# Performance work log

Measured on AMD Instinct MI355X. Metric: run time of the kernel, lower is better.

## Reference

```python
import jax, jax.numpy as jnp
import numpy as np

EMBED_DIM = 4096
NUM_HEADS = 32
NUM_KV_HEADS = 8
HEAD_DIM = EMBED_DIM // NUM_HEADS          # 128
Q_PER_KV = NUM_HEADS // NUM_KV_HEADS       # 4
KV_DIM = HEAD_DIM * NUM_KV_HEADS           # 1024
ROPE_BASE = 10000.0
ROTARY_DIM = HEAD_DIM                      # rotary_emb_dim = 128 (full head)


def setup_inputs() -> dict:
    key = jax.random.key(0)
    k1, k2, k3 = jax.random.split(key, 3)
    b, s = 2, 2048
    x = jax.random.normal(k1, (b, s, EMBED_DIM), dtype=jnp.float32)
    # torch nn.Linear weight layout: (out_features, in_features); scaled init
    wqkv_w = jax.random.normal(k2, (EMBED_DIM + 2 * KV_DIM, EMBED_DIM), dtype=jnp.float32) * (EMBED_DIM ** -0.5)
    wo_w = jax.random.normal(k3, (EMBED_DIM, EMBED_DIM), dtype=jnp.float32) * (EMBED_DIM ** -0.5)
    return {"x": x, "wqkv_w": wqkv_w, "wo_w": wo_w}


def _rope_cos_sin(seqlen, dtype):
    inv_freq = 1.0 / (ROPE_BASE ** (jnp.arange(0, ROTARY_DIM, 2, dtype=jnp.float32) / ROTARY_DIM))
    t = jnp.arange(seqlen, dtype=jnp.float32)
    freqs = jnp.outer(t, inv_freq)                 # (s, d/2)
    emb = jnp.concatenate([freqs, freqs], axis=-1)  # (s, d) — HF convention
    return jnp.cos(emb).astype(dtype), jnp.sin(emb).astype(dtype)


def _rotate_half(x):
    x1, x2 = jnp.split(x, 2, axis=-1)
    return jnp.concatenate([-x2, x1], axis=-1)


def _apply_rope(x, cos, sin):
    # x: (b, s, h, d); cos/sin: (s, d)
    c = cos[None, :, None, :]
    s_ = sin[None, :, None, :]
    return x * c + _rotate_half(x) * s_


def reference(x, wqkv_w, wo_w):
    b, s, _ = x.shape
    # packed QKV projection
    qkv = jnp.einsum("bse,fe->bsf", x, wqkv_w)
    # b s (h_kv * (q_per_kv + 2) * d) -> b s h_kv (q_per_kv+2) d
    qkv = qkv.reshape(b, s, NUM_KV_HEADS, Q_PER_KV + 2, HEAD_DIM)
    q = qkv[..., :Q_PER_KV, :].reshape(b, s, NUM_HEADS, HEAD_DIM)
    k = qkv[..., -2, :]   # (b, s, h_kv, d)
    v = qkv[..., -1, :]   # (b, s, h_kv, d)

    # RoPE (HF rotate_half impl, offsets = 0)
    cos, sin = _rope_cos_sin(s, x.dtype)
    q = _apply_rope(q, cos, sin)
    k = _apply_rope(k, cos, sin)

    # GQA: expand kv heads to match q heads
    k = jnp.repeat(k, Q_PER_KV, axis=2)   # (b, s, h, d)
    v = jnp.repeat(v, Q_PER_KV, axis=2)

    scale = HEAD_DIM ** -0.5
    scores = jnp.einsum("bqhd,bkhd->bhqk", q, k) * scale
    causal_mask = jnp.tril(jnp.ones((s, s), dtype=bool))
    scores = jnp.where(causal_mask[None, None], scores, jnp.finfo(scores.dtype).min)
    probs = jax.nn.softmax(scores, axis=-1)
    context = jnp.einsum("bhqk,bkhd->bqhd", probs, v)
    context = context.reshape(b, s, EMBED_DIM)
    return jnp.einsum("bse,fe->bsf", context, wo_w)
```

## Files before the change

### kernel.cpp

```cpp
#include <hip/hip_runtime.h>
#include <hip/hip_bf16.h>
#include <stdint.h>

typedef __hip_bfloat16 bf16;
typedef short bf16x8 __attribute__((ext_vector_type(8)));
typedef float f32x4 __attribute__((ext_vector_type(4)));

#define MFMA16(a, b, c) __builtin_amdgcn_mfma_f32_16x16x32_bf16((a), (b), (c), 0, 0, 0)

__device__ __forceinline__ void gload16(const void* g, void* l) {
  __builtin_amdgcn_global_load_lds((const __attribute__((address_space(1))) void*)g,
                                   (__attribute__((address_space(3))) void*)l,
                                   16, 0, 0);
}

__device__ __forceinline__ void stv(float* p, float v) { *p = v; }
__device__ __forceinline__ void stv(bf16* p, float v) { *p = __float2bfloat16(v); }

__global__ void cast_f32_bf16(const float* __restrict__ in, bf16* __restrict__ out,
                              long n) {
  const long stride = (long)gridDim.x * blockDim.x * 8;
  for (long i = ((long)blockIdx.x * blockDim.x + threadIdx.x) * 8; i < n; i += stride) {
    const float4 a = *(const float4*)&in[i];
    const float4 b = *(const float4*)&in[i + 4];
    bf16 t[8];
    t[0] = __float2bfloat16(a.x); t[1] = __float2bfloat16(a.y);
    t[2] = __float2bfloat16(a.z); t[3] = __float2bfloat16(a.w);
    t[4] = __float2bfloat16(b.x); t[5] = __float2bfloat16(b.y);
    t[6] = __float2bfloat16(b.z); t[7] = __float2bfloat16(b.w);
    *(bf16x8*)&out[i] = *(const bf16x8*)t;
  }
}

template <typename OutT>
__global__ __launch_bounds__(512, 2) void gemm256(const bf16* __restrict__ A,
                                                  const bf16* __restrict__ B,
                                                  OutT* __restrict__ C,
                                                  int M, int N, int K) {
  const int nbn = N >> 8;
  const int nwg = gridDim.x;
  const int wg = blockIdx.x;
  const int cpx = nwg >> 3;
  const int swz = (wg & 7) * cpx + (wg >> 3);
  const int bm = swz / nbn;
  const int bn = swz - bm * nbn;

  __shared__ bf16 As[2][256][64];
  __shared__ bf16 Bs[2][256][64];

  const int tid = threadIdx.x;
  const int wave = tid >> 6, lane = tid & 63;
  const int lo = lane & 15, hi = lane >> 4;
  const int wm = wave >> 2, wn = wave & 3;

  const bf16* Ag = A + (long)(bm * 256) * K;
  const bf16* Bg = B + (long)(bn * 256) * K;

  int srow[4]; int scol[4]; int sdst[4];
#pragma unroll
  for (int i = 0; i < 4; i++) {
    const int c = i * 512 + wave * 64 + lane;
    const int row = c >> 3, p = c & 7;
    srow[i] = row;
    scol[i] = (p ^ (row & 7)) * 8;
    sdst[i] = (i * 512 + wave * 64) * 8;
  }

  f32x4 acc[8][4] = {};
  const int NT = K >> 6;

#pragma unroll
  for (int p = 0; p < 2; p++) {
#pragma unroll
    for (int i = 0; i < 4; i++)
      gload16(Ag + (long)srow[i] * K + p * 64 + scol[i], &As[p][0][0] + sdst[i]);
#pragma unroll
    for (int i = 0; i < 4; i++)
      gload16(Bg + (long)srow[i] * K + p * 64 + scol[i], &Bs[p][0][0] + sdst[i]);
  }

#pragma unroll 1
  for (int t = 0; t < NT; ++t) {
    if (t >= NT - 1) asm volatile("s_waitcnt vmcnt(0)" ::: "memory");
    else             asm volatile("s_waitcnt vmcnt(8)" ::: "memory");
    __builtin_amdgcn_s_barrier();

    const bf16* Ab = &As[t & 1][0][0];
    const bf16* Bb = &Bs[t & 1][0][0];

#pragma unroll
    for (int ks = 0; ks < 2; ks++) {
      bf16x8 af[8], bfr[4];
#pragma unroll
      for (int m = 0; m < 8; m++) {
        const int row = wm * 128 + m * 16 + lo;
        af[m] = *(const bf16x8*)&Ab[row * 64 + ((ks * 4 + hi) ^ (lo & 7)) * 8];
      }
#pragma unroll
      for (int n = 0; n < 4; n++) {
        const int row = wn * 64 + n * 16 + lo;
        bfr[n] = *(const bf16x8*)&Bb[row * 64 + ((ks * 4 + hi) ^ (lo & 7)) * 8];
      }
      __builtin_amdgcn_s_setprio(1);
#pragma unroll
      for (int m = 0; m < 8; m++)
#pragma unroll
        for (int n = 0; n < 4; n++) acc[m][n] = MFMA16(af[m], bfr[n], acc[m][n]);
      __builtin_amdgcn_s_setprio(0);
    }

    asm volatile("s_waitcnt lgkmcnt(0)" ::: "memory");
    __builtin_amdgcn_s_barrier();

    if (t + 2 < NT) {
      const int kt = (t + 2) * 64;
      bf16* Ad = &As[t & 1][0][0];
      bf16* Bd = &Bs[t & 1][0][0];
#pragma unroll
      for (int i = 0; i < 4; i++)
        gload16(Ag + (long)srow[i] * K + kt + scol[i], Ad + sdst[i]);
#pragma unroll
      for (int i = 0; i < 4; i++)
        gload16(Bg + (long)srow[i] * K + kt + scol[i], Bd + sdst[i]);
    }
  }

  const long crow0 = (long)bm * 256 + wm * 128;
  const long ccol0 = (long)bn * 256 + wn * 64;
#pragma unroll
  for (int m = 0; m < 8; m++)
#pragma unroll
    for (int n = 0; n < 4; n++)
#pragma unroll
      for (int r = 0; r < 4; r++)
        stv(&C[(crow0 + m * 16 + hi * 4 + r) * (long)N + ccol0 + n * 16 + lo],
            acc[m][n][r]);
}

__global__ void rope_qk(bf16* __restrict__ qkv) {
  const int row = blockIdx.x;
  const int t = row & 2047;
  const float scale = 0.08838834764831845f;
  for (int p = threadIdx.x; p < 40 * 64; p += blockDim.x) {
    const int sh = p >> 6, j = p & 63;
    const int kvh = sh / 5, slot = sh - kvh * 5;
    const long base = (long)row * 6144 + kvh * 768 + slot * 128 + j;
    const float x1 = __bfloat162float(qkv[base]);
    const float x2 = __bfloat162float(qkv[base + 64]);
    const float inv = __expf(-(float)j * 0.14391156831212787f);
    const float ang = (float)t * inv;
    const float c = cosf(ang), s = sinf(ang);
    float o1 = x1 * c - x2 * s;
    float o2 = x2 * c + x1 * s;
    if (slot < 4) { o1 *= scale; o2 *= scale; }
    qkv[base] = __float2bfloat16(o1);
    qkv[base + 64] = __float2bfloat16(o2);
  }
}

__global__ void vtrans(const bf16* __restrict__ qkv, bf16* __restrict__ Vt) {
  const int tt = blockIdx.x, dd = blockIdx.y, bk = blockIdx.z;
  const int kvh = bk & 7, b = bk >> 3;
  __shared__ bf16 tile[64][65];
  const int tx = threadIdx.x, ty = threadIdx.y;
  const bf16* src = qkv + ((long)(b * 2048 + tt * 64)) * 6144 + kvh * 768 + 640 + dd * 64;
  for (int r = ty; r < 64; r += 4) tile[r][tx] = src[(long)r * 6144 + tx];
  __syncthreads();
  bf16* dst = Vt + ((long)bk * 128 + dd * 64) * 2048 + tt * 64;
  for (int r = ty; r < 64; r += 4) dst[(long)r * 2048 + tx] = tile[tx][r];
}

__global__ __launch_bounds__(256) void attn(const bf16* __restrict__ qkv,
                                            const bf16* __restrict__ Vt,
                                            bf16* __restrict__ Ctx) {
  const int lin = blockIdx.x;
  const int c = (lin & 7) * 64 + (lin >> 3);
  const int z = c & 31;
  const int kvh = (c >> 5) & 7;
  const int b = c >> 8;

  const int wave = threadIdx.x >> 6;
  const int lane = threadIdx.x & 63;
  const int h = kvh * 4 + wave;
  const int lo = lane & 15, hi = lane >> 4;

  const bf16* Qb = qkv + (long)b * 2048 * 6144 + kvh * 768 + wave * 128;
  const bf16* Kb = qkv + (long)b * 2048 * 6144 + kvh * 768 + 512;
  const bf16* Vb = Vt + ((long)(b * 8 + kvh)) * 128 * 2048;

  __shared__ bf16 Plds[4][32][40];

#pragma unroll 1
  for (int pass = 0; pass < 2; ++pass) {
    const int qw = pass ? 63 - z : z;
    const int q0 = qw * 32;

    bf16x8 qf[2][4];
#pragma unroll
    for (int qb = 0; qb < 2; qb++)
#pragma unroll
      for (int dc = 0; dc < 4; dc++)
        qf[qb][dc] =
            *(const bf16x8*)&Qb[(long)(q0 + qb * 16 + lo) * 6144 + dc * 32 + hi * 8];

    f32x4 acc[2][8] = {};
    float mrow[2][4], lrow[2][4];
#pragma unroll
    for (int qb = 0; qb < 2; qb++)
#pragma unroll
      for (int r = 0; r < 4; r++) {
        mrow[qb][r] = -1e30f;
        lrow[qb][r] = 0.0f;
      }

    for (int kt = 0; kt <= qw; ++kt) {
      const int k0 = kt * 32;
      f32x4 sacc[2][2] = {};
      __builtin_amdgcn_s_setprio(1);
#pragma unroll
      for (int kb = 0; kb < 2; kb++)
#pragma unroll
        for (int dc = 0; dc < 4; dc++) {
          const bf16x8 kf =
              *(const bf16x8*)&Kb[(long)(k0 + kb * 16 + lo) * 6144 + dc * 32 + hi * 8];
          sacc[0][kb] = MFMA16(qf[0][dc], kf, sacc[0][kb]);
          sacc[1][kb] = MFMA16(qf[1][dc], kf, sacc[1][kb]);
        }
      __builtin_amdgcn_s_setprio(0);

      if (kt == qw) {
#pragma unroll
        for (int qb = 0; qb < 2; qb++)
#pragma unroll
          for (int kb = 0; kb < 2; kb++) {
            const int q = q0 + qb * 16 + hi * 4;
            const int k = k0 + kb * 16 + lo;
#pragma unroll
            for (int r = 0; r < 4; r++)
              if (k > q + r) sacc[qb][kb][r] = -1e30f;
          }
      }

      float p[2][2][4];
      float sf[2][4];
#pragma unroll
      for (int qb = 0; qb < 2; qb++)
#pragma unroll
        for (int r = 0; r < 4; r++) {
          float pm = fmaxf(sacc[qb][0][r], sacc[qb][1][r]);
          pm = fmaxf(pm, __shfl_xor(pm, 1));
          pm = fmaxf(pm, __shfl_xor(pm, 2));
          pm = fmaxf(pm, __shfl_xor(pm, 4));
          pm = fmaxf(pm, __shfl_xor(pm, 8));
          const float mn = fmaxf(mrow[qb][r], pm);
          sf[qb][r] = __expf(mrow[qb][r] - mn);
          mrow[qb][r] = mn;
          float ps = 0.0f;
#pragma unroll
          for (int kb = 0; kb < 2; kb++) {
            p[qb][kb][r] = __expf(sacc[qb][kb][r] - mn);
            ps += p[qb][kb][r];
          }
          ps += __shfl_xor(ps, 1);
          ps += __shfl_xor(ps, 2);
          ps += __shfl_xor(ps, 4);
          ps += __shfl_xor(ps, 8);
          lrow[qb][r] = lrow[qb][r] * sf[qb][r] + ps;
        }

#pragma unroll
      for (int qb = 0; qb < 2; qb++)
#pragma unroll
        for (int dt = 0; dt < 8; dt++)
#pragma unroll
          for (int r = 0; r < 4; r++) acc[qb][dt][r] *= sf[qb][r];

#pragma unroll
      for (int qb = 0; qb < 2; qb++)
#pragma unroll
        for (int kb = 0; kb < 2; kb++)
#pragma unroll
          for (int r = 0; r < 4; r++)
            Plds[wave][qb * 16 + hi * 4 + r][kb * 16 + lo] = __float2bfloat16(p[qb][kb][r]);

      bf16x8 pa[2];
#pragma unroll
      for (int qb = 0; qb < 2; qb++)
        pa[qb] = *(const bf16x8*)&Plds[wave][qb * 16 + lo][hi * 8];

      __builtin_amdgcn_s_setprio(1);
#pragma unroll
      for (int dt = 0; dt < 8; dt++) {
        const bf16x8 vf = *(const bf16x8*)&Vb[(long)(dt * 16 + lo) * 2048 + k0 + hi * 8];
        acc[0][dt] = MFMA16(pa[0], vf, acc[0][dt]);
        acc[1][dt] = MFMA16(pa[1], vf, acc[1][dt]);
      }
      __builtin_amdgcn_s_setprio(0);
    }

#pragma unroll
    for (int qb = 0; qb < 2; qb++)
#pragma unroll
      for (int dt = 0; dt < 8; dt++)
#pragma unroll
        for (int r = 0; r < 4; r++) {
          const float o = acc[qb][dt][r] / lrow[qb][r];
          const long row = (long)b * 2048 + q0 + qb * 16 + hi * 4 + r;
          Ctx[row * 4096 + h * 128 + dt * 16 + lo] = __float2bfloat16(o);
        }
  }
}


extern "C" void kernel_launch(void* const* d_in, const int* in_sizes, int n_in,
                              void* d_out, int out_size, void* d_ws, size_t ws_size,
                              hipStream_t stream) {
  (void)in_sizes; (void)n_in; (void)out_size; (void)ws_size;
  const float* x = (const float*)d_in[0];
  const float* wqkv = (const float*)d_in[1];
  const float* wo = (const float*)d_in[2];
  float* out = (float*)d_out;

  const long NX = 4096L * 4096;
  const long NW1 = 6144L * 4096;

  const size_t XB_B = (size_t)NX * 2;
  const size_t WQ_B = (size_t)NW1 * 2;
  const size_t QKV_B = WQ_B;

  char* w = (char*)d_ws;
  bf16* xb = (bf16*)w;
  bf16* wqkvb = (bf16*)(w + XB_B);
  bf16* qkvp = (bf16*)(w + XB_B + WQ_B);
  bf16* Vtp = (bf16*)(w + XB_B + WQ_B + QKV_B);
  bf16* wob = xb;
  bf16* ctx = wqkvb;

  cast_f32_bf16<<<2048, 256, 0, stream>>>(x, xb, NX);
  cast_f32_bf16<<<2048, 256, 0, stream>>>(wqkv, wqkvb, NW1);

  gemm256<bf16><<<16 * 24, 512, 0, stream>>>(xb, wqkvb, qkvp, 4096, 6144, 4096);

  rope_qk<<<4096, 256, 0, stream>>>(qkvp);
  vtrans<<<dim3(32, 2, 16), dim3(64, 4), 0, stream>>>(qkvp, Vtp);

  cast_f32_bf16<<<2048, 256, 0, stream>>>(wo, wob, NX);

  attn<<<dim3(512), 256, 0, stream>>>(qkvp, Vtp, ctx);

  gemm256<float><<<16 * 16, 512, 0, stream>>>(ctx, wob, out, 4096, 4096, 4096);
}
```

Baseline: 728.5 us.

## Interleave GEMM global-to-LDS staging with four-phase MFMA clusters per K-tile

Reworks the bf16 GEMM main loop into four MFMA phases per 64-wide K tile. Each phase's LDS fragment reads overlap the issue of one half-tile global_load_lds, with barriers and sched_barriers between phases. The B tile for t+1 and the A tile for t+2 are staged on staggered schedules, and the vmcnt wait drops from 8 to 4. This is meant to spread memory traffic across the compute rather than bursting it after the MFMAs. The cost is more barriers per iteration and a subtle buffer-reuse ordering that could race if misordered.

Result: faster. 687.1 us (-5.7%).

```diff
diff --git a/kernel.cpp b/kernel.cpp
--- a/kernel.cpp
+++ b/kernel.cpp
@@ -56,74 +56,111 @@
   const bf16* Ag = A + (long)(bm * 256) * K;
   const bf16* Bg = B + (long)(bn * 256) * K;
 
-  int srow[4]; int scol[4]; int sdst[4];
-#pragma unroll
-  for (int i = 0; i < 4; i++) {
-    const int c = i * 512 + wave * 64 + lane;
-    const int row = c >> 3, p = c & 7;
-    srow[i] = row;
-    scol[i] = (p ^ (row & 7)) * 8;
-    sdst[i] = (i * 512 + wave * 64) * 8;
+  int srow[2], scol[2], sdst[2];
+#pragma unroll
+  for (int j = 0; j < 2; j++) {
+    const int c = j * 512 + tid;
+    const int row = c >> 3;
+    srow[j] = row;
+    scol[j] = ((c & 7) ^ (row & 7)) * 8;
+    sdst[j] = (j * 512 + wave * 64) * 8;
+  }
+
+#define STG(G, S, kt, h)                                                      \
+  {                                                                           \
+    _Pragma("unroll") for (int j = 0; j < 2; j++)                             \
+        gload16((G) + (long)((h)*128 + srow[j]) * K + (kt) + scol[j],         \
+                (S) + (h)*8192 + sdst[j]);                                    \
   }
 
   f32x4 acc[8][4] = {};
   const int NT = K >> 6;
 
-#pragma unroll
-  for (int p = 0; p < 2; p++) {
-#pragma unroll
-    for (int i = 0; i < 4; i++)
-      gload16(Ag + (long)srow[i] * K + p * 64 + scol[i], &As[p][0][0] + sdst[i]);
-#pragma unroll
-    for (int i = 0; i < 4; i++)
-      gload16(Bg + (long)srow[i] * K + p * 64 + scol[i], &Bs[p][0][0] + sdst[i]);
-  }
+  STG(Ag, &As[0][0][0], 0, 0); STG(Ag, &As[0][0][0], 0, 1);
+  STG(Bg, &Bs[0][0][0], 0, 0); STG(Bg, &Bs[0][0][0], 0, 1);
+  STG(Ag, &As[1][0][0], 64, 0); STG(Ag, &As[1][0][0], 64, 1);
 
 #pragma unroll 1
   for (int t = 0; t < NT; ++t) {
     if (t >= NT - 1) asm volatile("s_waitcnt vmcnt(0)" ::: "memory");
-    else             asm volatile("s_waitcnt vmcnt(8)" ::: "memory");
+    else             asm volatile("s_waitcnt vmcnt(4)" ::: "memory");
     __builtin_amdgcn_s_barrier();
 
     const bf16* Ab = &As[t & 1][0][0];
     const bf16* Bb = &Bs[t & 1][0][0];
-
-#pragma unroll
-    for (int ks = 0; ks < 2; ks++) {
-      bf16x8 af[8], bfr[4];
-#pragma unroll
-      for (int m = 0; m < 8; m++) {
-        const int row = wm * 128 + m * 16 + lo;
-        af[m] = *(const bf16x8*)&Ab[row * 64 + ((ks * 4 + hi) ^ (lo & 7)) * 8];
-      }
-#pragma unroll
-      for (int n = 0; n < 4; n++) {
-        const int row = wn * 64 + n * 16 + lo;
-        bfr[n] = *(const bf16x8*)&Bb[row * 64 + ((ks * 4 + hi) ^ (lo & 7)) * 8];
-      }
-      __builtin_amdgcn_s_setprio(1);
-#pragma unroll
-      for (int m = 0; m < 8; m++)
-#pragma unroll
-        for (int n = 0; n < 4; n++) acc[m][n] = MFMA16(af[m], bfr[n], acc[m][n]);
-      __builtin_amdgcn_s_setprio(0);
+    bf16* SAn = &As[t & 1][0][0];
+    bf16* SBn = &Bs[(t + 1) & 1][0][0];
+    const int kt1 = (t + 1) * 64, kt2 = (t + 2) * 64;
+    const bool s1 = (t + 1 < NT), s2 = (t + 2 < NT);
+    const int c0 = (hi ^ (lo & 7)) * 8;
+    const int c1 = ((4 + hi) ^ (lo & 7)) * 8;
+
+    bf16x8 a0[4], a1[4], a2[4], a3[4], b0[4], b1[4];
+
+#pragma unroll
+    for (int m = 0; m < 4; m++) {
+      const int row = (wm * 128 + m * 16 + lo) * 64;
+      a0[m] = *(const bf16x8*)&Ab[row + c0];
+      a1[m] = *(const bf16x8*)&Ab[row + c1];
     }
-
+#pragma unroll
+    for (int n = 0; n < 4; n++)
+      b0[n] = *(const bf16x8*)&Bb[(wn * 64 + n * 16 + lo) * 64 + c0];
+    if (s1) STG(Bg, SBn, kt1, 0);
+    __builtin_amdgcn_s_barrier();
     asm volatile("s_waitcnt lgkmcnt(0)" ::: "memory");
-    __builtin_amdgcn_s_barrier();
-
-    if (t + 2 < NT) {
-      const int kt = (t + 2) * 64;
-      bf16* Ad = &As[t & 1][0][0];
-      bf16* Bd = &Bs[t & 1][0][0];
-#pragma unroll
-      for (int i = 0; i < 4; i++)
-        gload16(Ag + (long)srow[i] * K + kt + scol[i], Ad + sdst[i]);
-#pragma unroll
-      for (int i = 0; i < 4; i++)
-        gload16(Bg + (long)srow[i] * K + kt + scol[i], Bd + sdst[i]);
+    __builtin_amdgcn_sched_barrier(0);
+    __builtin_amdgcn_s_setprio(1);
+#pragma unroll
+    for (int m = 0; m < 4; m++)
+#pragma unroll
+      for (int n = 0; n < 4; n++) acc[m][n] = MFMA16(a0[m], b0[n], acc[m][n]);
+    __builtin_amdgcn_s_setprio(0);
+    __builtin_amdgcn_s_barrier();
+
+#pragma unroll
+    for (int m = 0; m < 4; m++) {
+      const int row = (wm * 128 + 64 + m * 16 + lo) * 64;
+      a2[m] = *(const bf16x8*)&Ab[row + c0];
+      a3[m] = *(const bf16x8*)&Ab[row + c1];
     }
-  }
+    if (s1) STG(Bg, SBn, kt1, 1);
+    __builtin_amdgcn_s_barrier();
+    asm volatile("s_waitcnt lgkmcnt(0)" ::: "memory");
+    __builtin_amdgcn_sched_barrier(0);
+    __builtin_amdgcn_s_setprio(1);
+#pragma unroll
+    for (int m = 0; m < 4; m++)
+#pragma unroll
+      for (int n = 0; n < 4; n++) acc[4 + m][n] = MFMA16(a2[m], b0[n], acc[4 + m][n]);
+    __builtin_amdgcn_s_setprio(0);
+    __builtin_amdgcn_s_barrier();
+
+#pragma unroll
+    for (int n = 0; n < 4; n++)
+      b1[n] = *(const bf16x8*)&Bb[(wn * 64 + n * 16 + lo) * 64 + c1];
+    if (s2) STG(Ag, SAn, kt2, 0);
+    __builtin_amdgcn_s_barrier();
+    asm volatile("s_waitcnt lgkmcnt(0)" ::: "memory");
+    __builtin_amdgcn_sched_barrier(0);
+    __builtin_amdgcn_s_setprio(1);
+#pragma unroll
+    for (int m = 0; m < 4; m++)
+#pragma unroll
+      for (int n = 0; n < 4; n++) acc[m][n] = MFMA16(a1[m], b1[n], acc[m][n]);
+    __builtin_amdgcn_s_setprio(0);
+    __builtin_amdgcn_s_barrier();
+
+    if (s2) STG(Ag, SAn, kt2, 1);
+    __builtin_amdgcn_s_barrier();
+    __builtin_amdgcn_s_setprio(1);
+#pragma unroll
+    for (int m = 0; m < 4; m++)
+#pragma unroll
+      for (int n = 0; n < 4; n++) acc[4 + m][n] = MFMA16(a3[m], b1[n], acc[4 + m][n]);
+    __builtin_amdgcn_s_setprio(0);
+  }
+#undef STG
 
   const long crow0 = (long)bm * 256 + wm * 128;
   const long ccol0 = (long)bn * 256 + wn * 64;
```
